# Kernel tuning notes

Measured on AMD Instinct MI355X. Metric: run time of the kernel, lower is better.

The kernel has to match this reference:

```python
import jax, jax.numpy as jnp
from jax import lax
import numpy as np

B, Q, H, D = 4, 128, 32, 128
L = 4096
END = 1024  # cache_index: tokens already in cache


def setup_inputs() -> dict:
    key = jax.random.key(0)
    k1, k2, k3, k4, k5 = jax.random.split(key, 5)
    query = jax.random.normal(k1, (B, Q, H, D), jnp.float32)
    k_new = jax.random.normal(k2, (B, Q, H, D), jnp.float32)
    v_new = jax.random.normal(k3, (B, Q, H, D), jnp.float32)
    cache_key = jax.random.normal(k4, (B, L, H, D), jnp.float32)
    cache_value = jax.random.normal(k5, (B, L, H, D), jnp.float32)
    attention_mask = jnp.ones((B, L), dtype=jnp.bool_)
    # standard lower-triangular causal mask over the full cache length
    causal_mask = jnp.tril(jnp.ones((L, L), dtype=jnp.bool_))[None, None, :, :]
    return {
        "query": query,
        "key": k_new,
        "value": v_new,
        "cache_key": cache_key,
        "cache_value": cache_value,
        "attention_mask": attention_mask,
        "causal_mask": causal_mask,
        "cache_index": END,
    }


def reference(query, key, value, cache_key, cache_value, attention_mask, causal_mask, cache_index):
    """Faithful port of FlaxAttentionModule._concatenate_to_cache (quantizer = identity)."""
    b, q, h, d = query.shape
    max_length = cache_key.shape[1]
    dtype = query.dtype

    # attention_mask [B, L] -> [B, 1, 1, L]
    am = attention_mask[:, None, None, :]

    # slice causal mask rows for the current update window: [1, 1, q, L]
    cm = lax.dynamic_slice(causal_mask, (0, 0, cache_index, 0), (1, 1, q, max_length))
    cm = jnp.broadcast_to(cm, (b,) + cm.shape[1:])
    am = jnp.logical_and(jnp.broadcast_to(am, cm.shape), cm)

    # in-place cache update at the rotated write position
    slice_indices = (0, cache_index % max_length, 0, 0)
    value_cache = lax.dynamic_update_slice(cache_value, value.astype(cache_value.dtype), slice_indices)
    key_cache = lax.dynamic_update_slice(cache_key, key.astype(cache_key.dtype), slice_indices)

    # mask out not-yet-written cache slots
    pad_mask = jnp.broadcast_to(
        jnp.arange(max_length) < cache_index + q, (b, 1, q, max_length)
    )
    am = jnp.logical_and(pad_mask, am)

    # init_attention_bias(): 0 where attended, dtype-min elsewhere
    bias = jnp.where(
        am,
        jnp.zeros((), dtype),
        jnp.full((), jnp.finfo(dtype).min, dtype),
    )
    return key_cache, value_cache, bias
```

## Files before the change

### kernel.cpp

```cpp
#include <hip/hip_runtime.h>

#define B_BATCH 4
#define Q_NEW   128
#define H_HEADS 32
#define D_HEAD  128
#define L_CACHE 4096

#define NTHREADS 524288
#define CACHE_F4 16777216
#define ITERS    32

typedef float f4 __attribute__((ext_vector_type(4)));
using mask_t = unsigned char;

__global__ __launch_bounds__(256) void fused_cache_bias_kernel(
    const f4* __restrict__ key_new,
    const f4* __restrict__ val_new,
    const f4* __restrict__ cache_key,
    const f4* __restrict__ cache_val,
    f4* __restrict__ out_key,
    f4* __restrict__ out_val,
    const mask_t* __restrict__ att,
    const mask_t* __restrict__ causal,
    f4* __restrict__ bias_out,
    const int* __restrict__ cache_index_p)
{
    const int tid = blockIdx.x * 256 + threadIdx.x;
    const int ci  = *cache_index_p;

    int start = ci % L_CACHE;
    if (start < 0) start = 0;
    if (start > L_CACHE - Q_NEW) start = L_CACHE - Q_NEW;

    {
        int crow = ci;
        if (crow < 0) crow = 0;
        if (crow > L_CACHE - Q_NEW) crow = L_CACHE - Q_NEW;

        const int j4   = tid & (L_CACHE / 4 - 1);
        const int rowi = tid >> 10;
        const int qi   = rowi & (Q_NEW - 1);
        const int b    = rowi >> 7;

        const uchar4 a4 = *(const uchar4*)(att + b * L_CACHE + j4 * 4);
        const uchar4 c4 = *(const uchar4*)(causal + (long)(crow + qi) * L_CACHE + j4 * 4);

        const int jb        = j4 * 4;
        const int pad_limit = ci + Q_NEW;
        const float NEG = __int_as_float(0xFF7F7FFF);

        f4 o;
        o.x = (a4.x && c4.x && (jb + 0) < pad_limit) ? 0.0f : NEG;
        o.y = (a4.y && c4.y && (jb + 1) < pad_limit) ? 0.0f : NEG;
        o.z = (a4.z && c4.z && (jb + 2) < pad_limit) ? 0.0f : NEG;
        o.w = (a4.w && c4.w && (jb + 3) < pad_limit) ? 0.0f : NEG;
        __builtin_nontemporal_store(o, &bias_out[tid]);
    }

#pragma unroll 8
    for (int t = 0; t < ITERS; ++t) {
        const int i   = tid + t * NTHREADS;
        const int row = i >> 10;
        const int l   = row & (L_CACHE - 1);
        const int rel = l - start;
        const bool use_new = (unsigned)rel < (unsigned)Q_NEW;

        const int b   = row >> 12;
        const int src = ((b * Q_NEW + rel) << 10) | (i & 1023);

        const f4* kp = use_new ? (key_new + src) : (cache_key + i);
        const f4* vp = use_new ? (val_new + src) : (cache_val + i);

        const f4 k = __builtin_nontemporal_load(kp);
        const f4 v = __builtin_nontemporal_load(vp);
        __builtin_nontemporal_store(k, &out_key[i]);
        __builtin_nontemporal_store(v, &out_val[i]);
    }
}

extern "C" void kernel_launch(void* const* d_in, const int* in_sizes, int n_in,
                              void* d_out, int out_size, void* d_ws, size_t ws_size,
                              hipStream_t stream) {
    const f4*     key_new   = (const f4*)d_in[1];
    const f4*     val_new   = (const f4*)d_in[2];
    const f4*     cache_key = (const f4*)d_in[3];
    const f4*     cache_val = (const f4*)d_in[4];
    const mask_t* att       = (const mask_t*)d_in[5];
    const mask_t* causal    = (const mask_t*)d_in[6];
    const int*    cache_idx = (const int*)d_in[7];

    float* out = (float*)d_out;
    const long cache_elems = (long)B_BATCH * L_CACHE * H_HEADS * D_HEAD;
    f4* out_key  = (f4*)(out);
    f4* out_val  = (f4*)(out + cache_elems);
    f4* bias_out = (f4*)(out + 2 * cache_elems);

    fused_cache_bias_kernel<<<2048, 256, 0, stream>>>(
        key_new, val_new, cache_key, cache_val, out_key, out_val,
        att, causal, bias_out, cache_idx);
}
```

Baseline: 200.9 us.

## Split cache copy from new-token overwrite and bias into two kernels

The fused kernel is split in two. The first kernel does a pure streaming copy of the whole key and value caches, with no per-element selection. The second kernel then overwrites the Q new rows and writes the bias. This removes the per-element branch and address selection from the bulk copy, but it adds a second launch and writes the overwritten rows twice, which is extra traffic.

```diff
diff --git a/kernel.cpp b/kernel.cpp
--- a/kernel.cpp
+++ b/kernel.cpp
@@ -13,11 +13,28 @@
 typedef float f4 __attribute__((ext_vector_type(4)));
 using mask_t = unsigned char;
 
-__global__ __launch_bounds__(256) void fused_cache_bias_kernel(
+__global__ __launch_bounds__(256) void pure_copy_kernel(
+    const f4* __restrict__ cache_key,
+    const f4* __restrict__ cache_val,
+    f4* __restrict__ out_key,
+    f4* __restrict__ out_val)
+{
+    const int tid = blockIdx.x * 256 + threadIdx.x;
+#pragma unroll 8
+    for (int t = 0; t < ITERS; ++t) {
+        const int i = tid + t * NTHREADS;
+        __builtin_nontemporal_store(__builtin_nontemporal_load(&cache_key[i]), &out_key[i]);
+    }
+#pragma unroll 8
+    for (int t = 0; t < ITERS; ++t) {
+        const int i = tid + t * NTHREADS;
+        __builtin_nontemporal_store(__builtin_nontemporal_load(&cache_val[i]), &out_val[i]);
+    }
+}
+
+__global__ __launch_bounds__(256) void update_bias_kernel(
     const f4* __restrict__ key_new,
     const f4* __restrict__ val_new,
-    const f4* __restrict__ cache_key,
-    const f4* __restrict__ cache_val,
     f4* __restrict__ out_key,
     f4* __restrict__ out_val,
     const mask_t* __restrict__ att,
@@ -28,9 +45,20 @@
     const int tid = blockIdx.x * 256 + threadIdx.x;
     const int ci  = *cache_index_p;
 
-    int start = ci % L_CACHE;
-    if (start < 0) start = 0;
-    if (start > L_CACHE - Q_NEW) start = L_CACHE - Q_NEW;
+    {
+        int start = ci % L_CACHE;
+        if (start < 0) start = 0;
+        if (start > L_CACHE - Q_NEW) start = L_CACHE - Q_NEW;
+
+        const int col = tid & 1023;
+        const int r   = tid >> 10;
+        const int b   = r >> 7;
+        const int q   = r & (Q_NEW - 1);
+        const int dst = ((b * L_CACHE + start + q) << 10) | col;
+
+        __builtin_nontemporal_store(__builtin_nontemporal_load(&key_new[tid]), &out_key[dst]);
+        __builtin_nontemporal_store(__builtin_nontemporal_load(&val_new[tid]), &out_val[dst]);
+    }
 
     {
         int crow = ci;
@@ -56,26 +84,6 @@
         o.w = (a4.w && c4.w && (jb + 3) < pad_limit) ? 0.0f : NEG;
         __builtin_nontemporal_store(o, &bias_out[tid]);
     }
-
-#pragma unroll 8
-    for (int t = 0; t < ITERS; ++t) {
-        const int i   = tid + t * NTHREADS;
-        const int row = i >> 10;
-        const int l   = row & (L_CACHE - 1);
-        const int rel = l - start;
-        const bool use_new = (unsigned)rel < (unsigned)Q_NEW;
-
-        const int b   = row >> 12;
-        const int src = ((b * Q_NEW + rel) << 10) | (i & 1023);
-
-        const f4* kp = use_new ? (key_new + src) : (cache_key + i);
-        const f4* vp = use_new ? (val_new + src) : (cache_val + i);
-
-        const f4 k = __builtin_nontemporal_load(kp);
-        const f4 v = __builtin_nontemporal_load(vp);
-        __builtin_nontemporal_store(k, &out_key[i]);
-        __builtin_nontemporal_store(v, &out_val[i]);
-    }
 }
 
 extern "C" void kernel_launch(void* const* d_in, const int* in_sizes, int n_in,
@@ -95,7 +103,8 @@
     f4* out_val  = (f4*)(out + cache_elems);
     f4* bias_out = (f4*)(out + 2 * cache_elems);
 
-    fused_cache_bias_kernel<<<2048, 256, 0, stream>>>(
-        key_new, val_new, cache_key, cache_val, out_key, out_val,
-        att, causal, bias_out, cache_idx);
+    pure_copy_kernel<<<2048, 256, 0, stream>>>(cache_key, cache_val, out_key, out_val);
+
+    update_bias_kernel<<<2048, 256, 0, stream>>>(
+        key_new, val_new, out_key, out_val, att, causal, bias_out, cache_idx);
 }
```

Result: slower. 238.3 us (+18.6%).
